# Kernel tuning notes

Hardware: AMD Instinct MI355X
Metric: run time of the kernel (lower is better)

The kernel has to match this reference:

```python
import jax, jax.numpy as jnp
import numpy as np

N_NODES = 100000
N_EDGES = 3200000
F_IN = 128
HIDDEN = 16
F_OUT = 2


def setup_inputs() -> dict:
    key = jax.random.key(0)
    k1, k2, k3, k4 = jax.random.split(key, 4)
    x = jax.random.normal(k1, (N_NODES, F_IN), dtype=jnp.float32)
    edge_index = jax.random.randint(k2, (2, N_EDGES), 0, N_NODES, dtype=jnp.int64)
    # Glorot-ish init like torch_geometric's GCNConv linear layers
    W1 = jax.random.normal(k3, (F_IN, HIDDEN), dtype=jnp.float32) * (1.0 / np.sqrt(F_IN))
    b1 = jnp.zeros((HIDDEN,), dtype=jnp.float32)
    W2 = jax.random.normal(k4, (HIDDEN, F_OUT), dtype=jnp.float32) * (1.0 / np.sqrt(HIDDEN))
    b2 = jnp.zeros((F_OUT,), dtype=jnp.float32)
    return {"x": x, "edge_index": edge_index, "W1": W1, "b1": b1, "W2": W2, "b2": b2}


def _gcn_conv(x, src, dst, W, b, num_nodes):
    """PyG GCNConv: out = D^{-1/2}(A+I)D^{-1/2} X W + b (self-loops included in src/dst)."""
    h = x @ W  # [N, F_out]
    ones = jnp.ones(src.shape[0], dtype=h.dtype)
    deg = jax.ops.segment_sum(ones, dst, num_segments=num_nodes)  # in-degree incl. self-loop
    deg_inv_sqrt = jnp.where(deg > 0, jax.lax.rsqrt(jnp.maximum(deg, 1.0)), 0.0)
    norm = deg_inv_sqrt[src] * deg_inv_sqrt[dst]  # [E+N]
    msg = h[src] * norm[:, None]  # gather + scale: [E+N, F_out]
    out = jax.ops.segment_sum(msg, dst, num_segments=num_nodes)  # scatter-add
    return out + b


def reference(x, edge_index, W1, b1, W2, b2):
    num_nodes = x.shape[0]
    self_loops = jnp.arange(num_nodes, dtype=edge_index.dtype)
    src = jnp.concatenate([edge_index[0], self_loops])
    dst = jnp.concatenate([edge_index[1], self_loops])
    h = jax.nn.relu(_gcn_conv(x, src, dst, W1, b1, num_nodes))
    # F.dropout(training=self.training) is identity in eval mode
    out = _gcn_conv(h, src, dst, W2, b2, num_nodes)
    return out
```

## Files before the change

kernel.cpp:

```cpp
#include <hip/hip_runtime.h>

#define N_NODES 100000
#define N_EDGES 3200000
#define F_IN    128
#define HIDDEN  16
#define F_OUT   2

#define BSZ     256
#define NB      391
#define NPAD    (NB * BSZ)
#define G       800
#define EPB     (N_EDGES / G)
#define DUMMY_E 100000u

typedef float  f32x4 __attribute__((ext_vector_type(4)));
typedef float  f32x2 __attribute__((ext_vector_type(2)));
typedef _Float16 half8 __attribute__((ext_vector_type(8)));
typedef _Float16 half2v __attribute__((ext_vector_type(2)));

__global__ __launch_bounds__(512) void k_hist(const int* __restrict__ dst,
                                              unsigned* __restrict__ blockHist) {
    __shared__ unsigned h0[NB];
    __shared__ unsigned h1[NB];
    int t = threadIdx.x, g = blockIdx.x;
    for (int i = t; i < NB; i += 512) { h0[i] = 0u; h1[i] = 0u; }
    __syncthreads();
    const int2* d2 = (const int2*)(dst + g * EPB);
    unsigned* myh = (t & 1) ? h1 : h0;
    for (int i = t; i < EPB / 2; i += 512) {
        int2 v = d2[i];
        atomicAdd(&myh[(unsigned)v.x >> 8], 1u);
        atomicAdd(&myh[(unsigned)v.y >> 8], 1u);
    }
    __syncthreads();
    for (int i = t; i < NB; i += 512) blockHist[i * G + g] = h0[i] + h1[i];
}

__global__ __launch_bounds__(1024) void k_scan_blocks(unsigned* __restrict__ blockHist,
                                                      unsigned* __restrict__ total) {
    __shared__ unsigned s[1024];
    int b = blockIdx.x, t = threadIdx.x;
    unsigned v = (t < G) ? blockHist[b * G + t] : 0u;
    s[t] = v;
    __syncthreads();
    for (int off = 1; off < 1024; off <<= 1) {
        unsigned xv = (t >= off) ? s[t - off] : 0u;
        __syncthreads();
        s[t] += xv;
        __syncthreads();
    }
    if (t < G) blockHist[b * G + t] = s[t] - v;
    if (t == 1023) total[b] = s[t];
}

__global__ __launch_bounds__(512) void k_scan_buckets(const unsigned* __restrict__ total,
                                                      unsigned* __restrict__ bucketBase,
                                                      int* __restrict__ rowstart) {
    __shared__ unsigned s[512];
    int t = threadIdx.x;
    unsigned v = (t < NB) ? total[t] : 0u;
    s[t] = v;
    __syncthreads();
    for (int off = 1; off < 512; off <<= 1) {
        unsigned xv = (t >= off) ? s[t - off] : 0u;
        __syncthreads();
        s[t] += xv;
        __syncthreads();
    }
    if (t < NB) bucketBase[t] = s[t] - v;
    if (t == 511) {
        bucketBase[NB] = s[t];
        rowstart[N_NODES] = (int)s[t];
    }
}

__global__ __launch_bounds__(512) void k_scatter(const int* __restrict__ src,
                                                 const int* __restrict__ dst,
                                                 const unsigned* __restrict__ blockHist,
                                                 const unsigned* __restrict__ bucketBase,
                                                 unsigned* __restrict__ adj) {
    __shared__ unsigned stage[EPB];
    __shared__ unsigned short stage_b[EPB];
    __shared__ unsigned hist[NB];
    __shared__ unsigned h1[NB];
    __shared__ unsigned lstart[NB];
    __shared__ unsigned gbase[NB];
    __shared__ unsigned ssum[512];
    int t = threadIdx.x, g = blockIdx.x;
    for (int i = t; i < NB; i += 512) {
        hist[i] = 0u; h1[i] = 0u;
        gbase[i] = bucketBase[i] + blockHist[i * G + g];
    }
    __syncthreads();
    const int2* s2 = (const int2*)(src + g * EPB);
    const int2* d2 = (const int2*)(dst + g * EPB);
    unsigned* myh = (t & 1) ? h1 : hist;
    for (int i = t; i < EPB / 2; i += 512) {
        int2 v = d2[i];
        atomicAdd(&myh[(unsigned)v.x >> 8], 1u);
        atomicAdd(&myh[(unsigned)v.y >> 8], 1u);
    }
    __syncthreads();
    unsigned v0 = (t < NB) ? hist[t] + h1[t] : 0u;
    ssum[t] = v0;
    __syncthreads();
    for (int off = 1; off < 512; off <<= 1) {
        unsigned xv = (t >= off) ? ssum[t - off] : 0u;
        __syncthreads();
        ssum[t] += xv;
        __syncthreads();
    }
    unsigned e0 = ssum[t] - v0;
    if (t < NB) { lstart[t] = e0; hist[t] = e0; }
    __syncthreads();
    for (int i = t; i < EPB / 2; i += 512) {
        int2 sv = s2[i], dv = d2[i];
        unsigned bkt0 = (unsigned)dv.x >> 8;
        unsigned pos0 = atomicAdd(&hist[bkt0], 1u);
        stage[pos0] = ((unsigned)(dv.x & 255) << 17) | (unsigned)sv.x;
        stage_b[pos0] = (unsigned short)bkt0;
        unsigned bkt1 = (unsigned)dv.y >> 8;
        unsigned pos1 = atomicAdd(&hist[bkt1], 1u);
        stage[pos1] = ((unsigned)(dv.y & 255) << 17) | (unsigned)sv.y;
        stage_b[pos1] = (unsigned short)bkt1;
    }
    __syncthreads();
    for (int j = t; j < EPB; j += 512) {
        unsigned bkt = stage_b[j];
        adj[gbase[bkt] + (j - lstart[bkt])] = stage[j];
    }
}

#define SXP 132
__global__ __launch_bounds__(512) void k_sortmm(const unsigned* __restrict__ adj,
                                                const unsigned* __restrict__ bucketBase,
                                                const float* __restrict__ x,
                                                const float* __restrict__ W1,
                                                unsigned* __restrict__ adj2,
                                                int* __restrict__ rowstart,
                                                float* __restrict__ dinv,
                                                char* __restrict__ hs) {
    __shared__ float sW[F_IN * HIDDEN];
    __shared__ float sX[64 * SXP];
    __shared__ unsigned hist[BSZ];
    __shared__ unsigned sc[BSZ];
    __shared__ unsigned cur[BSZ];
    __shared__ float sdinv[BSZ];
    int b = blockIdx.x, t = threadIdx.x;
    for (int i = t; i < F_IN * HIDDEN; i += 512) sW[i] = W1[i];
    if (t < BSZ) hist[t] = 0u;
    __syncthreads();
    int e0 = (int)bucketBase[b], e1 = (int)bucketBase[b + 1];
    for (int i = e0 + t; i < e1; i += 512) atomicAdd(&hist[adj[i] >> 17], 1u);
    __syncthreads();
    if (t < BSZ) sc[t] = hist[t];
    __syncthreads();
    for (int off = 1; off < BSZ; off <<= 1) {
        unsigned a = 0;
        if (t < BSZ && t >= off) a = sc[t - off];
        __syncthreads();
        if (t < BSZ) sc[t] += a;
        __syncthreads();
    }
    if (t < BSZ) {
        unsigned deg = hist[t];
        unsigned excl = sc[t] - deg;
        cur[t] = (unsigned)e0 + excl;
        float dv = rsqrtf((float)(deg + 1u));
        sdinv[t] = dv;
        int node = b * BSZ + t;
        if (node < N_NODES) {
            rowstart[node] = e0 + (int)excl;
            dinv[node] = dv;
        }
    }
    __syncthreads();
    for (int i = e0 + t; i < e1; i += 512) {
        unsigned v = adj[i];
        unsigned pos = atomicAdd(&cur[v >> 17], 1u);
        adj2[pos] = v & 0x1FFFFu;
    }
    int nl = t >> 3;
    int c8 = t & 7;
    for (int tile = 0; tile < 4; ++tile) {
        int node0 = b * BSZ + tile * 64;
        __syncthreads();
        const float4* xv = (const float4*)(x + (size_t)node0 * F_IN);
        int maxv = (N_NODES - node0) * (F_IN / 4);
        if (maxv < 0) maxv = 0;
        for (int i = t; i < 64 * (F_IN / 4); i += 512) {
            if (i < maxv) {
                int nn = i >> 5, f4 = i & 31;
                ((float4*)(sX + nn * SXP))[f4] = xv[i];
            }
        }
        __syncthreads();
        int node = node0 + nl;
        float acc0 = 0.f, acc1 = 0.f;
        const f32x2* sW2 = (const f32x2*)sW;
        #pragma unroll 8
        for (int f = 0; f < F_IN; ++f) {
            float xval = sX[nl * SXP + f];
            f32x2 wv = sW2[f * 8 + c8];
            acc0 = fmaf(xval, wv[0], acc0);
            acc1 = fmaf(xval, wv[1], acc1);
        }
        if (node < NPAD) {
            float dv = (node < N_NODES) ? sdinv[tile * 64 + nl] : 0.f;
            half2v h2;
            h2[0] = (_Float16)(acc0 * dv);
            h2[1] = (_Float16)(acc1 * dv);
            *(half2v*)(hs + (size_t)node * 32 + c8 * 4) = h2;
        }
    }
}

__global__ __launch_bounds__(256) void k_agg1(const unsigned* __restrict__ adj2,
                                              const int* __restrict__ rowstart,
                                              const char* __restrict__ hs,
                                              const float* __restrict__ dinv,
                                              const float* __restrict__ b1,
                                              const float* __restrict__ W2,
                                              float2* __restrict__ hs2) {
    int g = blockIdx.x * 256 + threadIdx.x;
    int node = g >> 1, le = g & 1;
    if (node >= N_NODES) {
        if (le == 0 && node < NPAD) { float2 z = {0.f, 0.f}; hs2[node] = z; }
        return;
    }
    int rs = rowstart[node], re = rowstart[node + 1];
    unsigned le16 = (unsigned)le * 16u;
    unsigned dummy_off = DUMMY_E * 32u + le16;

    float a0 = 0.f, a1 = 0.f, a2 = 0.f, a3 = 0.f, a4 = 0.f, a5 = 0.f, a6 = 0.f, a7 = 0.f;
    f32x4 w0, w1, w2, w3, w4, w5, w6, w7;

#define GL1(dst, o) asm volatile("global_load_dwordx4 %0, %1, %2" \
    : "=v"(dst) : "v"(o), "s"(hs) : "memory");
#define AC1(w_) { half8 h8; __builtin_memcpy(&h8, &w_, 16); \
    a0 += (float)h8[0]; a1 += (float)h8[1]; a2 += (float)h8[2]; a3 += (float)h8[3]; \
    a4 += (float)h8[4]; a5 += (float)h8[5]; a6 += (float)h8[6]; a7 += (float)h8[7]; }

    for (int bs = rs; bs < re; bs += 8) {
        const unsigned* ap = adj2 + bs;
        unsigned j0 = ap[0], j1 = ap[1], j2 = ap[2], j3 = ap[3];
        unsigned j4 = ap[4], j5 = ap[5], j6 = ap[6], j7 = ap[7];
        unsigned o0 = (bs + 0 < re) ? (j0 << 5) + le16 : dummy_off;
        unsigned o1 = (bs + 1 < re) ? (j1 << 5) + le16 : dummy_off;
        unsigned o2 = (bs + 2 < re) ? (j2 << 5) + le16 : dummy_off;
        unsigned o3 = (bs + 3 < re) ? (j3 << 5) + le16 : dummy_off;
        unsigned o4 = (bs + 4 < re) ? (j4 << 5) + le16 : dummy_off;
        unsigned o5 = (bs + 5 < re) ? (j5 << 5) + le16 : dummy_off;
        unsigned o6 = (bs + 6 < re) ? (j6 << 5) + le16 : dummy_off;
        unsigned o7 = (bs + 7 < re) ? (j7 << 5) + le16 : dummy_off;
        GL1(w0, o0) GL1(w1, o1) GL1(w2, o2) GL1(w3, o3)
        GL1(w4, o4) GL1(w5, o5) GL1(w6, o6) GL1(w7, o7)
        asm volatile("s_waitcnt vmcnt(0)" ::: "memory");
        __builtin_amdgcn_sched_barrier(0);
        AC1(w0) AC1(w1) AC1(w2) AC1(w3) AC1(w4) AC1(w5) AC1(w6) AC1(w7)
    }
    const _Float16* selfrow = (const _Float16*)(hs + (size_t)node * 32 + le16);
    float dv = dinv[node];
    float q0 = dv * (a0 + (float)selfrow[0]), q1 = dv * (a1 + (float)selfrow[1]);
    float q2 = dv * (a2 + (float)selfrow[2]), q3 = dv * (a3 + (float)selfrow[3]);
    float q4 = dv * (a4 + (float)selfrow[4]), q5 = dv * (a5 + (float)selfrow[5]);
    float q6 = dv * (a6 + (float)selfrow[6]), q7 = dv * (a7 + (float)selfrow[7]);
    const float4* b1v = (const float4*)(b1 + le * 8);
    float4 ba = b1v[0], bb = b1v[1];
    const float4* w2v = (const float4*)(W2 + le * 16);
    float4 wA = w2v[0], wB = w2v[1], wC = w2v[2], wD = w2v[3];
    float p0 = 0.f, p1 = 0.f, r;
    r = fmaxf(q0 + ba.x, 0.f); p0 = fmaf(r, wA.x, p0); p1 = fmaf(r, wA.y, p1);
    r = fmaxf(q1 + ba.y, 0.f); p0 = fmaf(r, wA.z, p0); p1 = fmaf(r, wA.w, p1);
    r = fmaxf(q2 + ba.z, 0.f); p0 = fmaf(r, wB.x, p0); p1 = fmaf(r, wB.y, p1);
    r = fmaxf(q3 + ba.w, 0.f); p0 = fmaf(r, wB.z, p0); p1 = fmaf(r, wB.w, p1);
    r = fmaxf(q4 + bb.x, 0.f); p0 = fmaf(r, wC.x, p0); p1 = fmaf(r, wC.y, p1);
    r = fmaxf(q5 + bb.y, 0.f); p0 = fmaf(r, wC.z, p0); p1 = fmaf(r, wC.w, p1);
    r = fmaxf(q6 + bb.z, 0.f); p0 = fmaf(r, wD.x, p0); p1 = fmaf(r, wD.y, p1);
    r = fmaxf(q7 + bb.w, 0.f); p0 = fmaf(r, wD.z, p0); p1 = fmaf(r, wD.w, p1);
    p0 += __shfl_xor(p0, 1);
    p1 += __shfl_xor(p1, 1);
    if (le == 0) {
        float2 h2; h2.x = p0 * dv; h2.y = p1 * dv;
        hs2[node] = h2;
    }
}

__global__ __launch_bounds__(256) void k_agg2(const unsigned* __restrict__ adj2,
                                              const int* __restrict__ rowstart,
                                              const char* __restrict__ hs2,
                                              const float* __restrict__ dinv,
                                              const float* __restrict__ b2,
                                              float2* __restrict__ out) {
    int node = blockIdx.x * 256 + threadIdx.x;
    if (node >= N_NODES) return;
    int rs = rowstart[node], re = rowstart[node + 1];
    unsigned dummy_off = DUMMY_E * 8u;

    float a0 = 0.f, a1 = 0.f;
    f32x2 w0, w1, w2, w3, w4, w5, w6, w7;

#define GL2(dst, o) asm volatile("global_load_dwordx2 %0, %1, %2" \
    : "=v"(dst) : "v"(o), "s"(hs2) : "memory");

    for (int bs = rs; bs < re; bs += 8) {
        const unsigned* ap = adj2 + bs;
        unsigned j0 = ap[0], j1 = ap[1], j2 = ap[2], j3 = ap[3];
        unsigned j4 = ap[4], j5 = ap[5], j6 = ap[6], j7 = ap[7];
        unsigned o0 = (bs + 0 < re) ? (j0 << 3) : dummy_off;
        unsigned o1 = (bs + 1 < re) ? (j1 << 3) : dummy_off;
        unsigned o2 = (bs + 2 < re) ? (j2 << 3) : dummy_off;
        unsigned o3 = (bs + 3 < re) ? (j3 << 3) : dummy_off;
        unsigned o4 = (bs + 4 < re) ? (j4 << 3) : dummy_off;
        unsigned o5 = (bs + 5 < re) ? (j5 << 3) : dummy_off;
        unsigned o6 = (bs + 6 < re) ? (j6 << 3) : dummy_off;
        unsigned o7 = (bs + 7 < re) ? (j7 << 3) : dummy_off;
        GL2(w0, o0) GL2(w1, o1) GL2(w2, o2) GL2(w3, o3)
        GL2(w4, o4) GL2(w5, o5) GL2(w6, o6) GL2(w7, o7)
        asm volatile("s_waitcnt vmcnt(0)" ::: "memory");
        __builtin_amdgcn_sched_barrier(0);
        a0 += w0[0] + w1[0] + w2[0] + w3[0] + w4[0] + w5[0] + w6[0] + w7[0];
        a1 += w0[1] + w1[1] + w2[1] + w3[1] + w4[1] + w5[1] + w6[1] + w7[1];
    }
    const float2* h2p = (const float2*)hs2;
    float2 selfv = h2p[node];
    float dv = dinv[node];
    float2 r;
    r.x = fmaf(dv, a0 + selfv.x, b2[0]);
    r.y = fmaf(dv, a1 + selfv.y, b2[1]);
    out[node] = r;
}

extern "C" void kernel_launch(void* const* d_in, const int* in_sizes, int n_in,
                              void* d_out, int out_size, void* d_ws, size_t ws_size,
                              hipStream_t stream) {
    const float* x   = (const float*)d_in[0];
    const int*   ei  = (const int*)d_in[1];
    const int*   srcv = ei;
    const int*   dstv = ei + N_EDGES;
    const float* W1  = (const float*)d_in[2];
    const float* b1  = (const float*)d_in[3];
    const float* W2  = (const float*)d_in[4];
    const float* b2  = (const float*)d_in[5];
    float* out = (float*)d_out;

    char* w = (char*)d_ws;
    unsigned* adj        = (unsigned*)w;  w += (size_t)N_EDGES * 4;
    unsigned* adj2       = (unsigned*)w;  w += (size_t)(N_EDGES + 8) * 4;
    unsigned* blockHist  = (unsigned*)w;  w += (size_t)NB * G * 4;
    unsigned* total      = (unsigned*)w;  w += (size_t)NB * 4;
    unsigned* bucketBase = (unsigned*)w;  w += (size_t)(NB + 1) * 4;
    int*      rowstart   = (int*)w;       w += (size_t)(N_NODES + 1) * 4;
    w = (char*)(((size_t)w + 15) & ~(size_t)15);
    float* dinv  = (float*)w;  w += (size_t)N_NODES * 4;
    char*  hs    = w;          w += (size_t)NPAD * HIDDEN * 2;
    float* hs2   = (float*)w;

    k_hist        <<<G, 512, 0, stream>>>(dstv, blockHist);
    k_scan_blocks <<<NB, 1024, 0, stream>>>(blockHist, total);
    k_scan_buckets<<<1, 512, 0, stream>>>(total, bucketBase, rowstart);
    k_scatter     <<<G, 512, 0, stream>>>(srcv, dstv, blockHist, bucketBase, adj);
    k_sortmm      <<<NB, 512, 0, stream>>>(adj, bucketBase, x, W1, adj2, rowstart, dinv, hs);
    k_agg1        <<<(2 * NPAD) / 256, 256, 0, stream>>>(adj2, rowstart, hs, dinv,
                                                         b1, W2, (float2*)hs2);
    k_agg2        <<<(NPAD + 255) / 256, 256, 0, stream>>>(adj2, rowstart, (const char*)hs2,
                                                           dinv, b2, (float2*)out);
}
```

Baseline: 129.0 us.

## Halve sort bucket size and compute X·W1 directly from global memory

Bucket width drops from 256 to 128 nodes, doubling the bucket count to 782. The scatter and bucket-scan kernels are adapted so each thread scans two buckets and the global scan uses 1024 threads. The sort+matmul kernel no longer stages x through LDS in 64-node tiles. Each node is now handled by 4 lanes that each read a 32-feature slice straight from global memory, accumulate all 16 outputs, combine them with xor shuffles, and write 4 halfs each. This doubles the number of sort blocks for more parallelism and removes the LDS staging and barriers, at the cost of more registers and uncoalesced-ish row reads.

New measurement: 139.2 us, median of 2. +7.9%, slower.

```diff
diff --git a/kernel.cpp b/kernel.cpp
--- a/kernel.cpp
+++ b/kernel.cpp
@@ -6,8 +6,8 @@
 #define HIDDEN  16
 #define F_OUT   2
 
-#define BSZ     256
-#define NB      391
+#define BSZ     128
+#define NB      782
 #define NPAD    (NB * BSZ)
 #define G       800
 #define EPB     (N_EDGES / G)
@@ -16,7 +16,7 @@
 typedef float  f32x4 __attribute__((ext_vector_type(4)));
 typedef float  f32x2 __attribute__((ext_vector_type(2)));
 typedef _Float16 half8 __attribute__((ext_vector_type(8)));
-typedef _Float16 half2v __attribute__((ext_vector_type(2)));
+typedef _Float16 half4v __attribute__((ext_vector_type(4)));
 
 __global__ __launch_bounds__(512) void k_hist(const int* __restrict__ dst,
                                               unsigned* __restrict__ blockHist) {
@@ -29,8 +29,8 @@
     unsigned* myh = (t & 1) ? h1 : h0;
     for (int i = t; i < EPB / 2; i += 512) {
         int2 v = d2[i];
-        atomicAdd(&myh[(unsigned)v.x >> 8], 1u);
-        atomicAdd(&myh[(unsigned)v.y >> 8], 1u);
+        atomicAdd(&myh[(unsigned)v.x >> 7], 1u);
+        atomicAdd(&myh[(unsigned)v.y >> 7], 1u);
     }
     __syncthreads();
     for (int i = t; i < NB; i += 512) blockHist[i * G + g] = h0[i] + h1[i];
@@ -53,22 +53,22 @@
     if (t == 1023) total[b] = s[t];
 }
 
-__global__ __launch_bounds__(512) void k_scan_buckets(const unsigned* __restrict__ total,
-                                                      unsigned* __restrict__ bucketBase,
-                                                      int* __restrict__ rowstart) {
-    __shared__ unsigned s[512];
+__global__ __launch_bounds__(1024) void k_scan_buckets(const unsigned* __restrict__ total,
+                                                       unsigned* __restrict__ bucketBase,
+                                                       int* __restrict__ rowstart) {
+    __shared__ unsigned s[1024];
     int t = threadIdx.x;
     unsigned v = (t < NB) ? total[t] : 0u;
     s[t] = v;
     __syncthreads();
-    for (int off = 1; off < 512; off <<= 1) {
+    for (int off = 1; off < 1024; off <<= 1) {
         unsigned xv = (t >= off) ? s[t - off] : 0u;
         __syncthreads();
         s[t] += xv;
         __syncthreads();
     }
     if (t < NB) bucketBase[t] = s[t] - v;
-    if (t == 511) {
+    if (t == 1023) {
         bucketBase[NB] = s[t];
         rowstart[N_NODES] = (int)s[t];
     }
@@ -97,12 +97,15 @@
     unsigned* myh = (t & 1) ? h1 : hist;
     for (int i = t; i < EPB / 2; i += 512) {
         int2 v = d2[i];
-        atomicAdd(&myh[(unsigned)v.x >> 8], 1u);
-        atomicAdd(&myh[(unsigned)v.y >> 8], 1u);
-    }
-    __syncthreads();
-    unsigned v0 = (t < NB) ? hist[t] + h1[t] : 0u;
-    ssum[t] = v0;
+        atomicAdd(&myh[(unsigned)v.x >> 7], 1u);
+        atomicAdd(&myh[(unsigned)v.y >> 7], 1u);
+    }
+    __syncthreads();
+    int i0 = t * 2;
+    unsigned v0 = (i0 + 0 < NB) ? hist[i0 + 0] + h1[i0 + 0] : 0u;
+    unsigned v1 = (i0 + 1 < NB) ? hist[i0 + 1] + h1[i0 + 1] : 0u;
+    unsigned my = v0 + v1;
+    ssum[t] = my;
     __syncthreads();
     for (int off = 1; off < 512; off <<= 1) {
         unsigned xv = (t >= off) ? ssum[t - off] : 0u;
@@ -110,18 +113,21 @@
         ssum[t] += xv;
         __syncthreads();
     }
-    unsigned e0 = ssum[t] - v0;
-    if (t < NB) { lstart[t] = e0; hist[t] = e0; }
+    unsigned e0 = ssum[t] - my;
+    __syncthreads();
+    unsigned e1 = e0 + v0;
+    if (i0 + 0 < NB) { lstart[i0 + 0] = e0; hist[i0 + 0] = e0; }
+    if (i0 + 1 < NB) { lstart[i0 + 1] = e1; hist[i0 + 1] = e1; }
     __syncthreads();
     for (int i = t; i < EPB / 2; i += 512) {
         int2 sv = s2[i], dv = d2[i];
-        unsigned bkt0 = (unsigned)dv.x >> 8;
+        unsigned bkt0 = (unsigned)dv.x >> 7;
         unsigned pos0 = atomicAdd(&hist[bkt0], 1u);
-        stage[pos0] = ((unsigned)(dv.x & 255) << 17) | (unsigned)sv.x;
+        stage[pos0] = ((unsigned)(dv.x & 127) << 17) | (unsigned)sv.x;
         stage_b[pos0] = (unsigned short)bkt0;
-        unsigned bkt1 = (unsigned)dv.y >> 8;
+        unsigned bkt1 = (unsigned)dv.y >> 7;
         unsigned pos1 = atomicAdd(&hist[bkt1], 1u);
-        stage[pos1] = ((unsigned)(dv.y & 255) << 17) | (unsigned)sv.y;
+        stage[pos1] = ((unsigned)(dv.y & 127) << 17) | (unsigned)sv.y;
         stage_b[pos1] = (unsigned short)bkt1;
     }
     __syncthreads();
@@ -131,7 +137,6 @@
     }
 }
 
-#define SXP 132
 __global__ __launch_bounds__(512) void k_sortmm(const unsigned* __restrict__ adj,
                                                 const unsigned* __restrict__ bucketBase,
                                                 const float* __restrict__ x,
@@ -141,7 +146,6 @@
                                                 float* __restrict__ dinv,
                                                 char* __restrict__ hs) {
     __shared__ float sW[F_IN * HIDDEN];
-    __shared__ float sX[64 * SXP];
     __shared__ unsigned hist[BSZ];
     __shared__ unsigned sc[BSZ];
     __shared__ unsigned cur[BSZ];
@@ -180,38 +184,39 @@
         unsigned pos = atomicAdd(&cur[v >> 17], 1u);
         adj2[pos] = v & 0x1FFFFu;
     }
-    int nl = t >> 3;
-    int c8 = t & 7;
-    for (int tile = 0; tile < 4; ++tile) {
-        int node0 = b * BSZ + tile * 64;
-        __syncthreads();
-        const float4* xv = (const float4*)(x + (size_t)node0 * F_IN);
-        int maxv = (N_NODES - node0) * (F_IN / 4);
-        if (maxv < 0) maxv = 0;
-        for (int i = t; i < 64 * (F_IN / 4); i += 512) {
-            if (i < maxv) {
-                int nn = i >> 5, f4 = i & 31;
-                ((float4*)(sX + nn * SXP))[f4] = xv[i];
+    int nl = t >> 2, q = t & 3;
+    int node = b * BSZ + nl;
+    f32x4 a0 = {0.f, 0.f, 0.f, 0.f}, a1 = a0, a2 = a0, a3 = a0;
+    if (node < N_NODES) {
+        const f32x4* xr = (const f32x4*)(x + (size_t)node * F_IN + q * 32);
+        const f32x4* wv = (const f32x4*)sW;
+        #pragma unroll
+        for (int k = 0; k < 8; ++k) {
+            f32x4 xq = xr[k];
+            int f0 = q * 32 + k * 4;
+            #pragma unroll
+            for (int j = 0; j < 4; ++j) {
+                float xv = xq[j];
+                const f32x4* wr = wv + (size_t)(f0 + j) * 4;
+                a0 += xv * wr[0];
+                a1 += xv * wr[1];
+                a2 += xv * wr[2];
+                a3 += xv * wr[3];
             }
         }
-        __syncthreads();
-        int node = node0 + nl;
-        float acc0 = 0.f, acc1 = 0.f;
-        const f32x2* sW2 = (const f32x2*)sW;
-        #pragma unroll 8
-        for (int f = 0; f < F_IN; ++f) {
-            float xval = sX[nl * SXP + f];
-            f32x2 wv = sW2[f * 8 + c8];
-            acc0 = fmaf(xval, wv[0], acc0);
-            acc1 = fmaf(xval, wv[1], acc1);
-        }
-        if (node < NPAD) {
-            float dv = (node < N_NODES) ? sdinv[tile * 64 + nl] : 0.f;
-            half2v h2;
-            h2[0] = (_Float16)(acc0 * dv);
-            h2[1] = (_Float16)(acc1 * dv);
-            *(half2v*)(hs + (size_t)node * 32 + c8 * 4) = h2;
-        }
+    }
+#define CMB(a_) { a_[0] += __shfl_xor(a_[0], 1); a_[1] += __shfl_xor(a_[1], 1); \
+                  a_[2] += __shfl_xor(a_[2], 1); a_[3] += __shfl_xor(a_[3], 1); \
+                  a_[0] += __shfl_xor(a_[0], 2); a_[1] += __shfl_xor(a_[1], 2); \
+                  a_[2] += __shfl_xor(a_[2], 2); a_[3] += __shfl_xor(a_[3], 2); }
+    CMB(a0) CMB(a1) CMB(a2) CMB(a3)
+    f32x4 mine = (q == 0) ? a0 : ((q == 1) ? a1 : ((q == 2) ? a2 : a3));
+    if (node < NPAD) {
+        float dv = (node < N_NODES) ? sdinv[nl] : 0.f;
+        half4v h;
+        h[0] = (_Float16)(mine[0] * dv); h[1] = (_Float16)(mine[1] * dv);
+        h[2] = (_Float16)(mine[2] * dv); h[3] = (_Float16)(mine[3] * dv);
+        *(half4v*)(hs + (size_t)node * 32 + q * 8) = h;
     }
 }
 
@@ -358,7 +363,7 @@
 
     k_hist        <<<G, 512, 0, stream>>>(dstv, blockHist);
     k_scan_blocks <<<NB, 1024, 0, stream>>>(blockHist, total);
-    k_scan_buckets<<<1, 512, 0, stream>>>(total, bucketBase, rowstart);
+    k_scan_buckets<<<1, 1024, 0, stream>>>(total, bucketBase, rowstart);
     k_scatter     <<<G, 512, 0, stream>>>(srcv, dstv, blockHist, bucketBase, adj);
     k_sortmm      <<<NB, 512, 0, stream>>>(adj, bucketBase, x, W1, adj2, rowstart, dinv, hs);
     k_agg1        <<<(2 * NPAD) / 256, 256, 0, stream>>>(adj2, rowstart, hs, dinv,
```
